# Optimization experiments

Hardware: AMD Instinct MI355X
Metric: run time of the kernel (lower is better)

Reference implementation:

```python
import math
import jax, jax.numpy as jnp
from jax import lax
import numpy as np

D = 128            # head_dim
B = 16             # independent KV streams (e.g., heads)
S = 4096           # update sequence length
P = 4096           # reconstruction positions
MAX_SEQ_LEN = 8192
# (n_waves, ema_rate, freq_low, freq_high) per level, coarse -> fine
LEVELS = [(16, 0.001, 0.01, 1.0), (32, 0.005, 0.5, 3.0), (64, 0.02, 1.0, 6.0), (128, 0.05, 2.0, 10.0), (256, 0.1, 4.0, 20.0)]
TWO_PI = 2.0 * math.pi


def setup_inputs() -> dict:
    key = jax.random.key(0)
    ks = jax.random.split(key, 2 + len(LEVELS))
    inp = {}
    inp['kv_vectors'] = jax.random.normal(ks[0], (B, S, D), dtype=jnp.float32)
    inp['positions'] = jnp.arange(S, dtype=jnp.int32)
    inp['recon_positions'] = jnp.sort(jax.random.randint(ks[1], (P,), 0, MAX_SEQ_LEN, dtype=jnp.int32))
    for i, (n, a, lo, hi) in enumerate(LEVELS):
        k1, k2 = jax.random.split(ks[2 + i], 2)
        inp[f'W_enc_{i}'] = jax.random.normal(k1, (3 * n, D), dtype=jnp.float32) / math.sqrt(D)
        inp[f'W_dec_{i}'] = jax.random.normal(k2, (D, n), dtype=jnp.float32) / math.sqrt(n)
        inp[f'base_freqs_{i}'] = jnp.linspace(lo, hi, n, dtype=jnp.float32)
    return inp


def _ema_final(x, alpha):
    # x: [S, ...]; returns EMA state after S sequential steps from zero init.
    def step(c, xt):
        return (1.0 - alpha) * c + alpha * xt, None
    final, _ = lax.scan(step, jnp.zeros(x.shape[1:], x.dtype), x)
    return final


def _forward(kv_vectors, positions, recon_positions, params):
    pos_norm = positions.astype(jnp.float32)[:, None] / MAX_SEQ_LEN    # [S,1]
    rpos_norm = recon_positions.astype(jnp.float32)[:, None] / MAX_SEQ_LEN  # [P,1]
    out = jnp.zeros((kv_vectors.shape[0], recon_positions.shape[0], D), jnp.float32)
    for (n, alpha, _lo, _hi), (W_enc, W_dec, base_freqs) in zip(LEVELS, params):
        deltas = jnp.einsum('bsd,wd->bsw', kv_vectors, W_enc)          # [B,S,3n]
        d_freq, d_amp, d_phase = jnp.split(deltas, 3, axis=-1)         # each [B,S,n]
        pos_signal = jnp.sin(base_freqs[None, :] * pos_norm * TWO_PI)  # [S,n]
        xs = jnp.stack([d_freq * pos_signal[None], jnp.abs(d_amp), d_phase], axis=0)  # [3,B,S,n]
        xs = jnp.transpose(xs, (2, 0, 1, 3))                           # [S,3,B,n]
        freqs, amps, phases = _ema_final(xs, alpha)                    # each [B,n]
        wave_phases = TWO_PI * (freqs[:, None, :] + base_freqs[None, None, :]) * rpos_norm[None] + phases[:, None, :]
        wave_values = amps[:, None, :] * jnp.sin(wave_phases)          # [B,P,n]
        out = out + jnp.einsum('bpn,dn->bpd', wave_values, W_dec)
    return out


def reference(kv_vectors, positions, recon_positions,
              W_enc_0, W_dec_0, base_freqs_0,
              W_enc_1, W_dec_1, base_freqs_1,
              W_enc_2, W_dec_2, base_freqs_2,
              W_enc_3, W_dec_3, base_freqs_3,
              W_enc_4, W_dec_4, base_freqs_4):
    params = [(W_enc_0, W_dec_0, base_freqs_0), (W_enc_1, W_dec_1, base_freqs_1),
              (W_enc_2, W_dec_2, base_freqs_2), (W_enc_3, W_dec_3, base_freqs_3),
              (W_enc_4, W_dec_4, base_freqs_4)]
    return _forward(kv_vectors, positions, recon_positions, params)
```

## Files before the change

kernel.cpp:

```cpp
#include <hip/hip_runtime.h>

typedef __attribute__((ext_vector_type(8))) short short8;
typedef __attribute__((ext_vector_type(4))) float floatx4;

#define NLEV 5
#define B_   16
#define S_   4096
#define D_   128
#define P_   4096
#define CTOT 496
#define BP   (B_ * CTOT)
#define WPADG 512
#define CENC 1488
#define INV2PI 0.15915494309189535f
#define NJBLK 336

__device__ __forceinline__ unsigned short f2bf(float f) {
    unsigned u = __float_as_uint(f);
    u += 0x7fffu + ((u >> 16) & 1u);
    return (unsigned short)(u >> 16);
}
__device__ __forceinline__ unsigned int pack2(float a, float b) {
    return (unsigned int)f2bf(a) | ((unsigned int)f2bf(b) << 16);
}

__global__ void pack_weights(const float* __restrict__ we0, const float* __restrict__ we1,
                             const float* __restrict__ we2, const float* __restrict__ we3,
                             const float* __restrict__ we4,
                             const float* __restrict__ wd0, const float* __restrict__ wd1,
                             const float* __restrict__ wd2, const float* __restrict__ wd3,
                             const float* __restrict__ wd4,
                             unsigned short* __restrict__ wencb,
                             unsigned short* __restrict__ wdbT,
                             float* __restrict__ accb)
{
    int idx = blockIdx.x * 256 + threadIdx.x;
    if (idx < 3 * BP) accb[idx] = 0.0f;
    const int NE = CENC * D_;
    if (idx < NE) {
        int c = idx >> 7, d = idx & 127;
        const float* src; int off;
        if (c < 48)        { src = we0; off = 0;   }
        else if (c < 144)  { src = we1; off = 48;  }
        else if (c < 336)  { src = we2; off = 144; }
        else               { src = (c < 720) ? we3 : we4; off = (c < 720) ? 336 : 720; }
        wencb[idx] = f2bf(src[(size_t)(c - off) * D_ + d]);
    } else {
        int k = idx - NE;
        if (k >= D_ * WPADG) return;
        int d = k >> 9, w = k & 511;
        float v = 0.0f;
        if (w < CTOT) {
            const float* src; int off, nl;
            if (w < 16)       { src = wd0; off = 0;   nl = 16;  }
            else if (w < 48)  { src = wd1; off = 16;  nl = 32;  }
            else if (w < 112) { src = wd2; off = 48;  nl = 64;  }
            else if (w < 240) { src = wd3; off = 112; nl = 128; }
            else              { src = wd4; off = 240; nl = 256; }
            v = src[(size_t)d * nl + (w - off)];
        }
        wdbT[k] = f2bf(v);
    }
}

__global__ __launch_bounds__(256) void encoder(
    const float* __restrict__ kv, const int* __restrict__ positions,
    const unsigned short* __restrict__ wencb,
    const float* __restrict__ bfr0, const float* __restrict__ bfr1,
    const float* __restrict__ bfr2, const float* __restrict__ bfr3,
    const float* __restrict__ bfr4,
    float* __restrict__ accb)
{
    __shared__ unsigned short kvb[64 * 136];
    __shared__ float pf[64];
    const int b   = blockIdx.y;
    const int bid = blockIdx.x;
    const int tid = threadIdx.x;

    int bx, lb;
    if (bid < 96)       { bx = bid / 24;            lb = bid % 24; }
    else if (bid < 144) { int r = bid - 96;  bx = 4 + r / 12; lb = r % 12; }
    else if (bid < 192) { int r = bid - 144; bx = 8 + r / 6;  lb = r % 6;  }
    else                { int r = bid - 192; bx = 16 + r / 3; lb = r % 3;  }
    const int t0 = S_ - 64 * (bx + 1);

    const float* src = kv + ((size_t)(b * S_ + t0)) * D_;
    #pragma unroll
    for (int f = 0; f < 8; ++f) {
        int idx = f * 256 + tid;
        int t = idx >> 5, d4 = idx & 31;
        float4 val = *(const float4*)(src + t * D_ + d4 * 4);
        unsigned long long u = (unsigned long long)pack2(val.x, val.y)
                             | ((unsigned long long)pack2(val.z, val.w) << 32);
        *(unsigned long long*)&kvb[t * 136 + d4 * 4] = u;
    }
    if (tid < 64) pf[tid] = (float)positions[t0 + tid] * (1.0f / 8192.0f);
    __syncthreads();

    const int wid = tid >> 6, lane = tid & 63, ln = lane & 15, quad = lane >> 4;

    const int cnt = 9 + (bx < 16 ? 12 : 0) + (bx < 8 ? 24 : 0) + (bx < 4 ? 48 : 0);
    int jid = lb * 4 + wid;
    if (jid >= cnt) return;

    const int   n_l[5]  = {16, 32, 64, 128, 256};
    const int   coff[5] = {0, 16, 48, 112, 240};
    const int   c3[5]   = {0, 48, 144, 336, 720};
    const float al[5]   = {0.001f, 0.005f, 0.02f, 0.05f, 0.1f};
    const float l2m[5]  = {-0.0014434169f, -0.0072315692f, -0.0291463449f,
                           -0.0740005794f, -0.1520030934f};
    const float* bfp[5] = {bfr0, bfr1, bfr2, bfr3, bfr4};

    int l = 0, ci = jid;
    {
        const int sz[5] = {3, 6, (bx < 16 ? 12 : 0), (bx < 8 ? 24 : 0), (bx < 4 ? 48 : 0)};
        #pragma unroll
        for (int q = 0; q < 4; ++q) {
            if (ci >= sz[l]) { ci -= sz[l]; ++l; }
        }
    }
    const int n = n_l[l];

    const unsigned short* wrow = wencb + (size_t)(c3[l] + ci * 16 + ln) * D_;
    floatx4 acc[4];
    #pragma unroll
    for (int m = 0; m < 4; ++m) acc[m] = (floatx4){0.f, 0.f, 0.f, 0.f};
    #pragma unroll
    for (int k = 0; k < 4; ++k) {
        short8 bfg = *(const short8*)(wrow + k * 32 + quad * 8);
        #pragma unroll
        for (int m = 0; m < 4; ++m) {
            short8 af = *(const short8*)&kvb[(m * 16 + ln) * 136 + k * 32 + quad * 8];
            acc[m] = __builtin_amdgcn_mfma_f32_16x16x32_bf16(af, bfg, acc[m], 0, 0, 0);
        }
    }

    const int kind  = (ci * 16) / n;
    const int local = ci * 16 + ln - kind * n;
    const float bsv = (kind == 0) ? bfp[l][local] : 0.0f;

    const float l2 = l2m[l];
    const float fs = exp2f(-l2);
    const float fq = exp2f(-(float)(quad * 4) * l2);
    const float em = exp2f(-16.0f * l2);
    float fr[4];
    fr[0] = fq; fr[1] = fq * fs; fr[2] = fr[1] * fs; fr[3] = fr[2] * fs;
    float Cm = al[l] * exp2f((float)(S_ - 1 - t0) * l2);

    float s = 0.0f;
    #pragma unroll
    for (int m = 0; m < 4; ++m) {
        #pragma unroll
        for (int r = 0; r < 4; ++r) {
            int   trel = m * 16 + quad * 4 + r;
            float wt   = Cm * fr[r];
            float v    = acc[m][r];
            if (kind == 0) {
                float rev = bsv * pf[trel];
                rev = __builtin_amdgcn_fractf(rev);
                v *= __builtin_amdgcn_sinf(rev);
            } else if (kind == 1) {
                v = fabsf(v);
            }
            s += wt * v;
        }
        Cm *= em;
    }
    s += __shfl_xor(s, 16);
    s += __shfl_xor(s, 32);
    if (lane < 16)
        atomicAdd(accb + (size_t)kind * BP + b * CTOT + coff[l] + local, s);
}

__global__ __launch_bounds__(256) void decoder(
    const float* __restrict__ accb,
    const unsigned short* __restrict__ wdbT, const int* __restrict__ rpos,
    const float* __restrict__ b0, const float* __restrict__ b1,
    const float* __restrict__ b2, const float* __restrict__ b3,
    const float* __restrict__ b4,
    float* __restrict__ out)
{
    __shared__ unsigned short v[64 * 264];
    __shared__ float rpn[64];
    const int b = blockIdx.y, p0 = blockIdx.x * 64, tid = threadIdx.x;
    if (tid < 64) rpn[tid] = (float)rpos[p0 + tid] * (1.0f / 8192.0f);

    const int wid = tid >> 6, lane = tid & 63, ln = lane & 15, quad = lane >> 4;
    const int nt0 = wid * 2;

    floatx4 acc[4][2];
    #pragma unroll
    for (int m = 0; m < 4; ++m)
        #pragma unroll
        for (int j = 0; j < 2; ++j) acc[m][j] = (floatx4){0.f, 0.f, 0.f, 0.f};

    #pragma unroll
    for (int half = 0; half < 2; ++half) {
        const int w0 = half * 256;
        const int w = w0 + tid;
        float A = 0.f, Q = 0.f, Ph = 0.f;
        if (w < CTOT) {
            const float* bf; int off;
            if (w < 16)       { bf = b0; off = 0;   }
            else if (w < 48)  { bf = b1; off = 16;  }
            else if (w < 112) { bf = b2; off = 48;  }
            else if (w < 240) { bf = b3; off = 112; }
            else              { bf = b4; off = 240; }
            float f  = accb[0 * BP + b * CTOT + w];
            A        = accb[1 * BP + b * CTOT + w];
            float ph = accb[2 * BP + b * CTOT + w];
            Q  = f + bf[w - off];
            Ph = ph * INV2PI;
        }
        __syncthreads();
        for (int p = 0; p < 64; p += 2) {
            float r0 = __builtin_amdgcn_fractf(fmaf(Q, rpn[p],     Ph));
            float r1 = __builtin_amdgcn_fractf(fmaf(Q, rpn[p + 1], Ph));
            float s0 = A * __builtin_amdgcn_sinf(r0);
            float s1 = A * __builtin_amdgcn_sinf(r1);
            unsigned pk;
            asm("v_cvt_pk_bf16_f32 %0, %1, %2" : "=v"(pk) : "v"(s0), "v"(s1));
            v[p * 264 + tid]       = (unsigned short)pk;
            v[(p + 1) * 264 + tid] = (unsigned short)(pk >> 16);
        }
        __syncthreads();

        #pragma unroll
        for (int kk = 0; kk < 8; ++kk) {
            short8 bn[2];
            #pragma unroll
            for (int j = 0; j < 2; ++j)
                bn[j] = *(const short8*)(wdbT + (size_t)((nt0 + j) * 16 + ln) * WPADG
                                         + w0 + kk * 32 + quad * 8);
            short8 am[4];
            #pragma unroll
            for (int m = 0; m < 4; ++m)
                am[m] = *(const short8*)&v[(m * 16 + ln) * 264 + kk * 32 + quad * 8];
            #pragma unroll
            for (int m = 0; m < 4; ++m)
                #pragma unroll
                for (int j = 0; j < 2; ++j)
                    acc[m][j] = __builtin_amdgcn_mfma_f32_16x16x32_bf16(
                                    am[m], bn[j], acc[m][j], 0, 0, 0);
        }
    }

    #pragma unroll
    for (int m = 0; m < 4; ++m)
        #pragma unroll
        for (int j = 0; j < 2; ++j)
            #pragma unroll
            for (int r = 0; r < 4; ++r) {
                int p = p0 + m * 16 + quad * 4 + r;
                int d = (nt0 + j) * 16 + ln;
                out[((size_t)(b * P_ + p)) * D_ + d] = acc[m][j][r];
            }
}

extern "C" void kernel_launch(void* const* d_in, const int* in_sizes, int n_in,
                              void* d_out, int out_size, void* d_ws, size_t ws_size,
                              hipStream_t stream)
{
    const float* kv        = (const float*)d_in[0];
    const int*   positions = (const int*)d_in[1];
    const int*   rpos      = (const int*)d_in[2];

    char* ws = (char*)d_ws;
    float*          accb  = (float*)(ws + 0);
    unsigned short* wencb = (unsigned short*)(ws + 95232);
    unsigned short* wdbT  = (unsigned short*)(ws + 476160);

    pack_weights<<<1000, 256, 0, stream>>>(
        (const float*)d_in[3], (const float*)d_in[6], (const float*)d_in[9],
        (const float*)d_in[12], (const float*)d_in[15],
        (const float*)d_in[4], (const float*)d_in[7], (const float*)d_in[10],
        (const float*)d_in[13], (const float*)d_in[16],
        wencb, wdbT, accb);

    encoder<<<dim3(NJBLK, B_), 256, 0, stream>>>(
        kv, positions, wencb,
        (const float*)d_in[5], (const float*)d_in[8], (const float*)d_in[11],
        (const float*)d_in[14], (const float*)d_in[17],
        accb);

    decoder<<<dim3(P_ / 64, B_), 256, 0, stream>>>(
        accb, wdbT, rpos,
        (const float*)d_in[5], (const float*)d_in[8], (const float*)d_in[11],
        (const float*)d_in[14], (const float*)d_in[17],
        (float*)d_out);
}
```

Measured before the change: 156.6 us.

## Fuse weight packing into encoder and replace atomics with per-chunk partial sums

Removes the separate pack_weights kernel: the encoder converts fp32 encoder weights to bf16 on the fly, and its first 64 blocks of batch 0 pack the decoder weights. Atomic accumulation into a pre-zeroed buffer is replaced by plain stores of per-time-chunk partials, which the decoder sums over a level-dependent number of chunks. This saves a launch and the zeroing pass, at the cost of redundant weight conversion in every encoder block and more partial reads in the decoder. The decoder relies on the encoder's wdbT writes, which is safe only because the two kernels run in order on the stream.

Result: slower. 174.7 us (+11.6%).

```diff
diff --git a/kernel.cpp b/kernel.cpp
--- a/kernel.cpp
+++ b/kernel.cpp
@@ -2,6 +2,7 @@
 
 typedef __attribute__((ext_vector_type(8))) short short8;
 typedef __attribute__((ext_vector_type(4))) float floatx4;
+typedef __attribute__((ext_vector_type(4))) int intx4;
 
 #define NLEV 5
 #define B_   16
@@ -10,46 +11,41 @@
 #define P_   4096
 #define CTOT 496
 #define BP   (B_ * CTOT)
+#define NBX  64
 #define WPADG 512
-#define CENC 1488
 #define INV2PI 0.15915494309189535f
 #define NJBLK 336
 
-__device__ __forceinline__ unsigned short f2bf(float f) {
-    unsigned u = __float_as_uint(f);
-    u += 0x7fffu + ((u >> 16) & 1u);
-    return (unsigned short)(u >> 16);
-}
-__device__ __forceinline__ unsigned int pack2(float a, float b) {
-    return (unsigned int)f2bf(a) | ((unsigned int)f2bf(b) << 16);
-}
-
-__global__ void pack_weights(const float* __restrict__ we0, const float* __restrict__ we1,
-                             const float* __restrict__ we2, const float* __restrict__ we3,
-                             const float* __restrict__ we4,
-                             const float* __restrict__ wd0, const float* __restrict__ wd1,
-                             const float* __restrict__ wd2, const float* __restrict__ wd3,
-                             const float* __restrict__ wd4,
-                             unsigned short* __restrict__ wencb,
-                             unsigned short* __restrict__ wdbT,
-                             float* __restrict__ accb)
+__device__ __forceinline__ unsigned cvtpk(float a, float b) {
+    unsigned r;
+    asm("v_cvt_pk_bf16_f32 %0, %1, %2" : "=v"(r) : "v"(a), "v"(b));
+    return r;
+}
+
+__global__ __launch_bounds__(256) void encoder(
+    const float* __restrict__ kv, const int* __restrict__ positions,
+    const float* __restrict__ we0, const float* __restrict__ we1,
+    const float* __restrict__ we2, const float* __restrict__ we3,
+    const float* __restrict__ we4,
+    const float* __restrict__ wd0, const float* __restrict__ wd1,
+    const float* __restrict__ wd2, const float* __restrict__ wd3,
+    const float* __restrict__ wd4,
+    const float* __restrict__ bfr0, const float* __restrict__ bfr1,
+    const float* __restrict__ bfr2, const float* __restrict__ bfr3,
+    const float* __restrict__ bfr4,
+    unsigned short* __restrict__ wdbT,
+    float* __restrict__ accb)
 {
-    int idx = blockIdx.x * 256 + threadIdx.x;
-    if (idx < 3 * BP) accb[idx] = 0.0f;
-    const int NE = CENC * D_;
-    if (idx < NE) {
-        int c = idx >> 7, d = idx & 127;
-        const float* src; int off;
-        if (c < 48)        { src = we0; off = 0;   }
-        else if (c < 144)  { src = we1; off = 48;  }
-        else if (c < 336)  { src = we2; off = 144; }
-        else               { src = (c < 720) ? we3 : we4; off = (c < 720) ? 336 : 720; }
-        wencb[idx] = f2bf(src[(size_t)(c - off) * D_ + d]);
-    } else {
-        int k = idx - NE;
-        if (k >= D_ * WPADG) return;
-        int d = k >> 9, w = k & 511;
-        float v = 0.0f;
+    __shared__ unsigned short kvb[64 * 136];
+    __shared__ float pf[64];
+    const int b   = blockIdx.y;
+    const int bid = blockIdx.x;
+    const int tid = threadIdx.x;
+
+    if (b == 0 && bid < 64) {
+        int e0 = (bid * 256 + tid) * 4;
+        int d = e0 >> 9, w = e0 & 511;
+        float4 v4 = {0.f, 0.f, 0.f, 0.f};
         if (w < CTOT) {
             const float* src; int off, nl;
             if (w < 16)       { src = wd0; off = 0;   nl = 16;  }
@@ -57,25 +53,12 @@
             else if (w < 112) { src = wd2; off = 48;  nl = 64;  }
             else if (w < 240) { src = wd3; off = 112; nl = 128; }
             else              { src = wd4; off = 240; nl = 256; }
-            v = src[(size_t)d * nl + (w - off)];
-        }
-        wdbT[k] = f2bf(v);
-    }
-}
-
-__global__ __launch_bounds__(256) void encoder(
-    const float* __restrict__ kv, const int* __restrict__ positions,
-    const unsigned short* __restrict__ wencb,
-    const float* __restrict__ bfr0, const float* __restrict__ bfr1,
-    const float* __restrict__ bfr2, const float* __restrict__ bfr3,
-    const float* __restrict__ bfr4,
-    float* __restrict__ accb)
-{
-    __shared__ unsigned short kvb[64 * 136];
-    __shared__ float pf[64];
-    const int b   = blockIdx.y;
-    const int bid = blockIdx.x;
-    const int tid = threadIdx.x;
+            v4 = *(const float4*)(src + (size_t)d * nl + (w - off));
+        }
+        *(unsigned long long*)&wdbT[e0] =
+            (unsigned long long)cvtpk(v4.x, v4.y)
+            | ((unsigned long long)cvtpk(v4.z, v4.w) << 32);
+    }
 
     int bx, lb;
     if (bid < 96)       { bx = bid / 24;            lb = bid % 24; }
@@ -90,9 +73,9 @@
         int idx = f * 256 + tid;
         int t = idx >> 5, d4 = idx & 31;
         float4 val = *(const float4*)(src + t * D_ + d4 * 4);
-        unsigned long long u = (unsigned long long)pack2(val.x, val.y)
-                             | ((unsigned long long)pack2(val.z, val.w) << 32);
-        *(unsigned long long*)&kvb[t * 136 + d4 * 4] = u;
+        *(unsigned long long*)&kvb[t * 136 + d4 * 4] =
+            (unsigned long long)cvtpk(val.x, val.y)
+            | ((unsigned long long)cvtpk(val.z, val.w) << 32);
     }
     if (tid < 64) pf[tid] = (float)positions[t0 + tid] * (1.0f / 8192.0f);
     __syncthreads();
@@ -105,11 +88,11 @@
 
     const int   n_l[5]  = {16, 32, 64, 128, 256};
     const int   coff[5] = {0, 16, 48, 112, 240};
-    const int   c3[5]   = {0, 48, 144, 336, 720};
     const float al[5]   = {0.001f, 0.005f, 0.02f, 0.05f, 0.1f};
     const float l2m[5]  = {-0.0014434169f, -0.0072315692f, -0.0291463449f,
                            -0.0740005794f, -0.1520030934f};
     const float* bfp[5] = {bfr0, bfr1, bfr2, bfr3, bfr4};
+    const float* wep[5] = {we0, we1, we2, we3, we4};
 
     int l = 0, ci = jid;
     {
@@ -121,13 +104,17 @@
     }
     const int n = n_l[l];
 
-    const unsigned short* wrow = wencb + (size_t)(c3[l] + ci * 16 + ln) * D_;
+    const float* wrow = wep[l] + (size_t)(ci * 16 + ln) * D_;
     floatx4 acc[4];
     #pragma unroll
     for (int m = 0; m < 4; ++m) acc[m] = (floatx4){0.f, 0.f, 0.f, 0.f};
     #pragma unroll
     for (int k = 0; k < 4; ++k) {
-        short8 bfg = *(const short8*)(wrow + k * 32 + quad * 8);
+        float4 wa = *(const float4*)(wrow + k * 32 + quad * 8);
+        float4 wb = *(const float4*)(wrow + k * 32 + quad * 8 + 4);
+        intx4 bi = { (int)cvtpk(wa.x, wa.y), (int)cvtpk(wa.z, wa.w),
+                     (int)cvtpk(wb.x, wb.y), (int)cvtpk(wb.z, wb.w) };
+        short8 bfg = *(short8*)&bi;
         #pragma unroll
         for (int m = 0; m < 4; ++m) {
             short8 af = *(const short8*)&kvb[(m * 16 + ln) * 136 + k * 32 + quad * 8];
@@ -169,7 +156,7 @@
     s += __shfl_xor(s, 16);
     s += __shfl_xor(s, 32);
     if (lane < 16)
-        atomicAdd(accb + (size_t)kind * BP + b * CTOT + coff[l] + local, s);
+        accb[((size_t)bx * 3 + kind) * BP + b * CTOT + coff[l] + local] = s;
 }
 
 __global__ __launch_bounds__(256) void decoder(
@@ -206,9 +193,16 @@
             else if (w < 112) { bf = b2; off = 48;  }
             else if (w < 240) { bf = b3; off = 112; }
             else              { bf = b4; off = 240; }
-            float f  = accb[0 * BP + b * CTOT + w];
-            A        = accb[1 * BP + b * CTOT + w];
-            float ph = accb[2 * BP + b * CTOT + w];
+            const int parts = (w < 48) ? 64 : (w < 112) ? 16 : (w < 240) ? 8 : 4;
+            float f = 0.f, Aa = 0.f, ph = 0.f;
+            const float* pp = accb + b * CTOT + w;
+            for (int x = 0; x < parts; ++x) {
+                f  += pp[0];
+                Aa += pp[BP];
+                ph += pp[2 * BP];
+                pp += 3 * (size_t)BP;
+            }
+            A  = Aa;
             Q  = f + bf[w - off];
             Ph = ph * INV2PI;
         }
@@ -218,8 +212,7 @@
             float r1 = __builtin_amdgcn_fractf(fmaf(Q, rpn[p + 1], Ph));
             float s0 = A * __builtin_amdgcn_sinf(r0);
             float s1 = A * __builtin_amdgcn_sinf(r1);
-            unsigned pk;
-            asm("v_cvt_pk_bf16_f32 %0, %1, %2" : "=v"(pk) : "v"(s0), "v"(s1));
+            unsigned pk = cvtpk(s0, s1);
             v[p * 264 + tid]       = (unsigned short)pk;
             v[(p + 1) * 264 + tid] = (unsigned short)(pk >> 16);
         }
@@ -267,21 +260,17 @@
 
     char* ws = (char*)d_ws;
     float*          accb  = (float*)(ws + 0);
-    unsigned short* wencb = (unsigned short*)(ws + 95232);
-    unsigned short* wdbT  = (unsigned short*)(ws + 476160);
-
-    pack_weights<<<1000, 256, 0, stream>>>(
+    unsigned short* wdbT  = (unsigned short*)(ws + 6094848);
+
+    encoder<<<dim3(NJBLK, B_), 256, 0, stream>>>(
+        kv, positions,
         (const float*)d_in[3], (const float*)d_in[6], (const float*)d_in[9],
         (const float*)d_in[12], (const float*)d_in[15],
         (const float*)d_in[4], (const float*)d_in[7], (const float*)d_in[10],
         (const float*)d_in[13], (const float*)d_in[16],
-        wencb, wdbT, accb);
-
-    encoder<<<dim3(NJBLK, B_), 256, 0, stream>>>(
-        kv, positions, wencb,
         (const float*)d_in[5], (const float*)d_in[8], (const float*)d_in[11],
         (const float*)d_in[14], (const float*)d_in[17],
-        accb);
+        wdbT, accb);
 
     decoder<<<dim3(P_ / 64, B_), 256, 0, stream>>>(
         accb, wdbT, rpos,
```

## Restructure decoder wave generation with swizzled LDS and prefetched weights

Applied to the files above, without the earlier changes.

The decoder now has each lane compute four consecutive waves for 16 positions and write 8-byte packed bf16 values into an XOR-swizzled shared-memory tile, replacing per-thread 2-byte scattered stores into a padded layout. The wave parameters are loaded once with float4 reads before the loop, and all decoder weight fragments for a half are prefetched into registers before the barrier. The encoder's manual bf16 rounding is replaced by the hardware packed conversion instruction. The intent is fewer LDS store instructions, fewer bank conflicts and hidden global-load latency, at the cost of extra register pressure from holding 16 weight fragments.

Result: no change. 158.0 us (+0.9%).

```diff
diff --git a/kernel.cpp b/kernel.cpp
--- a/kernel.cpp
+++ b/kernel.cpp
@@ -20,8 +20,10 @@
     u += 0x7fffu + ((u >> 16) & 1u);
     return (unsigned short)(u >> 16);
 }
-__device__ __forceinline__ unsigned int pack2(float a, float b) {
-    return (unsigned int)f2bf(a) | ((unsigned int)f2bf(b) << 16);
+__device__ __forceinline__ unsigned cvtpk(float a, float b) {
+    unsigned r;
+    asm("v_cvt_pk_bf16_f32 %0, %1, %2" : "=v"(r) : "v"(a), "v"(b));
+    return r;
 }
 
 __global__ void pack_weights(const float* __restrict__ we0, const float* __restrict__ we1,
@@ -90,9 +92,9 @@
         int idx = f * 256 + tid;
         int t = idx >> 5, d4 = idx & 31;
         float4 val = *(const float4*)(src + t * D_ + d4 * 4);
-        unsigned long long u = (unsigned long long)pack2(val.x, val.y)
-                             | ((unsigned long long)pack2(val.z, val.w) << 32);
-        *(unsigned long long*)&kvb[t * 136 + d4 * 4] = u;
+        *(unsigned long long*)&kvb[t * 136 + d4 * 4] =
+            (unsigned long long)cvtpk(val.x, val.y)
+            | ((unsigned long long)cvtpk(val.z, val.w) << 32);
     }
     if (tid < 64) pf[tid] = (float)positions[t0 + tid] * (1.0f / 8192.0f);
     __syncthreads();
@@ -180,13 +182,40 @@
     const float* __restrict__ b4,
     float* __restrict__ out)
 {
-    __shared__ unsigned short v[64 * 264];
+    __shared__ unsigned short v[64 * 256];
     __shared__ float rpn[64];
     const int b = blockIdx.y, p0 = blockIdx.x * 64, tid = threadIdx.x;
     if (tid < 64) rpn[tid] = (float)rpos[p0 + tid] * (1.0f / 8192.0f);
 
     const int wid = tid >> 6, lane = tid & 63, ln = lane & 15, quad = lane >> 4;
     const int nt0 = wid * 2;
+    char* vb = (char*)v;
+
+    float Qv[2][4], Av[2][4], Pv[2][4];
+    #pragma unroll
+    for (int h = 0; h < 2; ++h) {
+        const int wbase = h * 256 + lane * 4;
+        if (wbase < CTOT) {
+            const float* bf; int off;
+            if (wbase < 16)       { bf = b0; off = 0;   }
+            else if (wbase < 48)  { bf = b1; off = 16;  }
+            else if (wbase < 112) { bf = b2; off = 48;  }
+            else if (wbase < 240) { bf = b3; off = 112; }
+            else                  { bf = b4; off = 240; }
+            float4 ff = *(const float4*)(accb + 0 * BP + b * CTOT + wbase);
+            float4 aa = *(const float4*)(accb + 1 * BP + b * CTOT + wbase);
+            float4 pp = *(const float4*)(accb + 2 * BP + b * CTOT + wbase);
+            float4 bb = *(const float4*)(bf + (wbase - off));
+            Qv[h][0] = ff.x + bb.x; Qv[h][1] = ff.y + bb.y;
+            Qv[h][2] = ff.z + bb.z; Qv[h][3] = ff.w + bb.w;
+            Av[h][0] = aa.x; Av[h][1] = aa.y; Av[h][2] = aa.z; Av[h][3] = aa.w;
+            Pv[h][0] = pp.x * INV2PI; Pv[h][1] = pp.y * INV2PI;
+            Pv[h][2] = pp.z * INV2PI; Pv[h][3] = pp.w * INV2PI;
+        } else {
+            #pragma unroll
+            for (int j = 0; j < 4; ++j) { Qv[h][j] = 0.f; Av[h][j] = 0.f; Pv[h][j] = 0.f; }
+        }
+    }
 
     floatx4 acc[4][2];
     #pragma unroll
@@ -197,51 +226,52 @@
     #pragma unroll
     for (int half = 0; half < 2; ++half) {
         const int w0 = half * 256;
-        const int w = w0 + tid;
-        float A = 0.f, Q = 0.f, Ph = 0.f;
-        if (w < CTOT) {
-            const float* bf; int off;
-            if (w < 16)       { bf = b0; off = 0;   }
-            else if (w < 48)  { bf = b1; off = 16;  }
-            else if (w < 112) { bf = b2; off = 48;  }
-            else if (w < 240) { bf = b3; off = 112; }
-            else              { bf = b4; off = 240; }
-            float f  = accb[0 * BP + b * CTOT + w];
-            A        = accb[1 * BP + b * CTOT + w];
-            float ph = accb[2 * BP + b * CTOT + w];
-            Q  = f + bf[w - off];
-            Ph = ph * INV2PI;
-        }
+
+        short8 bn[8][2];
+        #pragma unroll
+        for (int kk = 0; kk < 8; ++kk)
+            #pragma unroll
+            for (int j = 0; j < 2; ++j)
+                bn[kk][j] = *(const short8*)(wdbT
+                             + (size_t)((nt0 + j) * 16 + ln) * WPADG
+                             + w0 + kk * 32 + quad * 8);
+
         __syncthreads();
-        for (int p = 0; p < 64; p += 2) {
-            float r0 = __builtin_amdgcn_fractf(fmaf(Q, rpn[p],     Ph));
-            float r1 = __builtin_amdgcn_fractf(fmaf(Q, rpn[p + 1], Ph));
-            float s0 = A * __builtin_amdgcn_sinf(r0);
-            float s1 = A * __builtin_amdgcn_sinf(r1);
-            unsigned pk;
-            asm("v_cvt_pk_bf16_f32 %0, %1, %2" : "=v"(pk) : "v"(s0), "v"(s1));
-            v[p * 264 + tid]       = (unsigned short)pk;
-            v[(p + 1) * 264 + tid] = (unsigned short)(pk >> 16);
+
+        const float Q0 = Qv[half][0], Q1 = Qv[half][1], Q2 = Qv[half][2], Q3 = Qv[half][3];
+        const float A0 = Av[half][0], A1 = Av[half][1], A2 = Av[half][2], A3 = Av[half][3];
+        const float P0 = Pv[half][0], P1 = Pv[half][1], P2 = Pv[half][2], P3 = Pv[half][3];
+        #pragma unroll 4
+        for (int pr = 0; pr < 16; ++pr) {
+            const int p = wid * 16 + pr;
+            const float rp = rpn[p];
+            float s0 = A0 * __builtin_amdgcn_sinf(__builtin_amdgcn_fractf(fmaf(Q0, rp, P0)));
+            float s1 = A1 * __builtin_amdgcn_sinf(__builtin_amdgcn_fractf(fmaf(Q1, rp, P1)));
+            float s2 = A2 * __builtin_amdgcn_sinf(__builtin_amdgcn_fractf(fmaf(Q2, rp, P2)));
+            float s3 = A3 * __builtin_amdgcn_sinf(__builtin_amdgcn_fractf(fmaf(Q3, rp, P3)));
+            unsigned long long u = (unsigned long long)cvtpk(s0, s1)
+                                 | ((unsigned long long)cvtpk(s2, s3) << 32);
+            int byte = p * 512 + lane * 8;
+            byte ^= (p & 7) << 4;
+            *(unsigned long long*)(vb + byte) = u;
         }
         __syncthreads();
 
         #pragma unroll
         for (int kk = 0; kk < 8; ++kk) {
-            short8 bn[2];
-            #pragma unroll
-            for (int j = 0; j < 2; ++j)
-                bn[j] = *(const short8*)(wdbT + (size_t)((nt0 + j) * 16 + ln) * WPADG
-                                         + w0 + kk * 32 + quad * 8);
             short8 am[4];
             #pragma unroll
-            for (int m = 0; m < 4; ++m)
-                am[m] = *(const short8*)&v[(m * 16 + ln) * 264 + kk * 32 + quad * 8];
+            for (int m = 0; m < 4; ++m) {
+                int byte = (m * 16 + ln) * 512 + kk * 64 + quad * 16;
+                byte ^= (ln & 7) << 4;
+                am[m] = *(const short8*)(vb + byte);
+            }
             #pragma unroll
             for (int m = 0; m < 4; ++m)
                 #pragma unroll
                 for (int j = 0; j < 2; ++j)
                     acc[m][j] = __builtin_amdgcn_mfma_f32_16x16x32_bf16(
-                                    am[m], bn[j], acc[m][j], 0, 0, 0);
+                                    am[m], bn[kk][j], acc[m][j], 0, 0, 0);
         }
     }
 
```
